# Kernel optimization log

Hardware: AMD Instinct MI355X
Metric: run time of the kernel (lower is better)

Reference implementation:

```python
import jax, jax.numpy as jnp
import numpy as np

N = 20000       # num_nodes
E = 200000      # ~ N*N*0.0005 directed edges from erdos_renyi
IN = 64         # in_channels
HID = 128       # hidden_channels (per head)
H = 4           # heads
OUT = 10        # out_channels
K1 = 10000      # ceil(0.5*N) nodes kept by pool1 (single graph -> static)
K2 = 5000       # ceil(0.5*K1) kept by pool2
NEG_SLOPE = 0.2 # PyG GATConv default negative_slope


def setup_inputs() -> dict:
    key = jax.random.key(0)
    ks = jax.random.split(key, 16)
    def glorot(k, shp, fan):
        return (jax.random.normal(k, shp, jnp.float32) / np.sqrt(fan)).astype(jnp.float32)
    x = jax.random.normal(ks[0], (N, IN), jnp.float32)
    edge_index = jax.random.randint(ks[1], (2, E), 0, N, dtype=jnp.int32)
    batch = jnp.zeros((N,), jnp.int32)
    W1 = glorot(ks[2], (IN, H * HID), IN)
    a_src1 = glorot(ks[3], (H, HID), HID)
    a_dst1 = glorot(ks[4], (H, HID), HID)
    b1 = jnp.zeros((H * HID,), jnp.float32)
    pw1 = glorot(ks[5], (H * HID,), H * HID)
    W2 = glorot(ks[6], (H * HID, H * HID), H * HID)
    a_src2 = glorot(ks[7], (H, HID), HID)
    a_dst2 = glorot(ks[8], (H, HID), HID)
    b2 = jnp.zeros((H * HID,), jnp.float32)
    pw2 = glorot(ks[9], (H * HID,), H * HID)
    Wl = glorot(ks[10], (H * HID, OUT), H * HID)
    bl = jnp.zeros((OUT,), jnp.float32)
    return dict(x=x, edge_index=edge_index, batch=batch,
                W1=W1, a_src1=a_src1, a_dst1=a_dst1, b1=b1, pw1=pw1,
                W2=W2, a_src2=a_src2, a_dst2=a_dst2, b2=b2, pw2=pw2,
                Wl=Wl, bl=bl)


def _gat(x, src, dst, emask, W, a_src, a_dst, bias):
    """PyG GATConv: gather -> LeakyReLU edge score -> scatter-softmax over dst -> scatter-add.
    Self-loops added (PyG default). emask marks valid edges (invalid edges point at node 0)."""
    n = x.shape[0]
    Hh, C = a_src.shape
    h = (x @ W).reshape(n, Hh, C)                      # [n,H,C]
    asrc = jnp.einsum('nhc,hc->nh', h, a_src)          # [n,H]
    adst = jnp.einsum('nhc,hc->nh', h, a_dst)
    loops = jnp.arange(n, dtype=src.dtype)
    sa = jnp.concatenate([src, loops])                 # [E+n]
    da = jnp.concatenate([dst, loops])
    ma = jnp.concatenate([emask, jnp.ones((n,), bool)])
    logit = jax.nn.leaky_relu(asrc[sa] + adst[da], negative_slope=NEG_SLOPE)  # [E+n,H]
    logit = jnp.where(ma[:, None], logit, -1e9)
    mx = jax.ops.segment_max(logit, da, num_segments=n)        # every node has a self-loop
    e = jnp.where(ma[:, None], jnp.exp(logit - mx[da]), 0.0)
    den = jax.ops.segment_sum(e, da, num_segments=n)
    alpha = e / den[da]                                         # [E+n,H]
    msg = (alpha[:, :, None] * h[sa]).reshape(-1, Hh * C)       # [E+n,H*C]
    return jax.ops.segment_sum(msg, da, num_segments=n) + bias  # concat heads + bias


def _topk_pool(x, src, dst, emask, w, k):
    """PyG TopKPooling (single graph): score = tanh(x.w/||w||), keep top-k nodes,
    scale kept features by score, relabel & mask edges between kept nodes."""
    score = jnp.tanh((x @ w) / jnp.linalg.norm(w))     # [n]
    vals, perm = jax.lax.top_k(score, k)
    xn = x[perm] * vals[:, None]                       # [k,F]
    remap = jnp.full((x.shape[0],), -1, jnp.int32).at[perm].set(jnp.arange(k, dtype=jnp.int32))
    s2 = remap[src]
    d2 = remap[dst]
    m2 = emask & (s2 >= 0) & (d2 >= 0)
    return xn, jnp.where(m2, s2, 0), jnp.where(m2, d2, 0), m2


def reference(x, edge_index, batch, W1, a_src1, a_dst1, b1, pw1,
              W2, a_src2, a_dst2, b2, pw2, Wl, bl):
    src = edge_index[0]
    dst = edge_index[1]
    mask = jnp.ones((src.shape[0],), bool)
    h = jax.nn.elu(_gat(x, src, dst, mask, W1, a_src1, a_dst1, b1))
    h, src, dst, mask = _topk_pool(h, src, dst, mask, pw1, K1)
    h = jax.nn.elu(_gat(h, src, dst, mask, W2, a_src2, a_dst2, b2))
    h, src, dst, mask = _topk_pool(h, src, dst, mask, pw2, K2)
    g = jnp.mean(h, axis=0, keepdims=True)             # global_mean_pool, single graph
    return g @ Wl + bl                                  # [1, OUT]
```

## Files before the change

kernel.cpp:

```cpp
#include <hip/hip_runtime.h>
#include <math.h>

#define N_NODES 20000
#define E_EDGES 200000
#define K1_KEEP 10000
#define K2_KEEP 5000
#define HIDC 128
#define NHEAD 4
#define FDIM 512
#define NEG 0.2f
#define BSTRIDE 64
#define MPAD 10112
#define MPAD1 20096
#define FR_GRID 250
#define FR_RPB 40
#define SSTRIDE 16

typedef _Float16 half8 __attribute__((ext_vector_type(8)));
typedef _Float16 half4 __attribute__((ext_vector_type(4)));
typedef float f32x4 __attribute__((ext_vector_type(4)));

__device__ __forceinline__ float leaky(float x){ return x > 0.f ? x : NEG * x; }
__device__ __forceinline__ float elu(float x){ return x > 0.f ? x : expm1f(x); }
__device__ __forceinline__ unsigned ordkey(float f){
    unsigned u = __float_as_uint(f);
    return (u & 0x80000000u) ? ~u : (u | 0x80000000u);
}

__global__ __launch_bounds__(256) void prep_x(const float* __restrict__ x,
        _Float16* __restrict__ X0, _Float16* __restrict__ X1)
{
    int tid = blockIdx.x * 256 + threadIdx.x;
    int r = tid >> 3, c8 = (tid & 7) << 3;
    half8 v0 = (half8)0, v1 = (half8)0;
    if (r < N_NODES){
        const float4* p = reinterpret_cast<const float4*>(&x[(size_t)r * 64 + c8]);
        float4 x0 = p[0], x1 = p[1];
        float vals[8] = {x0.x, x0.y, x0.z, x0.w, x1.x, x1.y, x1.z, x1.w};
#pragma unroll
        for (int j = 0; j < 8; ++j){
            _Float16 h = (_Float16)vals[j];
            v0[j] = h;
            v1[j] = (_Float16)(vals[j] - (float)h);
        }
    }
    *reinterpret_cast<half8*>(&X0[(size_t)r * 64 + c8]) = v0;
    *reinterpret_cast<half8*>(&X1[(size_t)r * 64 + c8]) = v1;
}

__global__ __launch_bounds__(256) void prep_w1x(const float* __restrict__ W1,
        _Float16* __restrict__ B0, _Float16* __restrict__ B1,
        int* __restrict__ ctmp, int cn,
        const float* __restrict__ cw, float* __restrict__ cinvn)
{
    int bid = blockIdx.x;
    int t = threadIdx.x;
    if (bid < 32){
        __shared__ float tile[32][33];
        int bn = bid & 15, bk = bid >> 4;
        int n0 = bn * 32, k0 = bk * 32;
        int j = t & 31, i0 = t >> 5;
#pragma unroll
        for (int ii = 0; ii < 32; ii += 8)
            tile[i0 + ii][j] = W1[(size_t)(k0 + i0 + ii) * 512 + n0 + j];
        __syncthreads();
#pragma unroll
        for (int ii = 0; ii < 32; ii += 8){
            float v = tile[j][i0 + ii];
            _Float16 h0 = (_Float16)v;
            _Float16 h1 = (_Float16)(v - (float)h0);
            size_t o = (size_t)(n0 + i0 + ii) * 64 + k0 + j;
            B0[o] = h0; B1[o] = h1;
        }
    } else if (bid < 32 + 79){
        int i = (bid - 32) * 256 + t;
        if (i < cn) ctmp[i] = 0;
    } else {
        __shared__ float redc[4];
        float s = cw[t] * cw[t] + cw[t + 256] * cw[t + 256];
#pragma unroll
        for (int off = 32; off > 0; off >>= 1) s += __shfl_xor(s, off);
        if ((t & 63) == 0) redc[t >> 6] = s;
        __syncthreads();
        if (t == 0) *cinvn = rsqrtf(redc[0] + redc[1] + redc[2] + redc[3]);
    }
}

__global__ __launch_bounds__(256) void prep_w2(const float* __restrict__ W2,
        _Float16* __restrict__ B0, _Float16* __restrict__ B1)
{
    __shared__ float tile[32][33];
    int bn = blockIdx.x & 15, bk = blockIdx.x >> 4;
    int n0 = bn * 32, k0 = bk * 32;
    int t = threadIdx.x;
    int j = t & 31, i0 = t >> 5;
#pragma unroll
    for (int ii = 0; ii < 32; ii += 8)
        tile[i0 + ii][j] = W2[(size_t)(k0 + i0 + ii) * 512 + n0 + j];
    __syncthreads();
#pragma unroll
    for (int ii = 0; ii < 32; ii += 8){
        float v = tile[j][i0 + ii];
        _Float16 h0 = (_Float16)v;
        _Float16 h1 = (_Float16)(v - (float)h0);
        size_t o = (size_t)(n0 + i0 + ii) * 512 + k0 + j;
        B0[o] = h0; B1[o] = h1;
    }
}

__global__ __launch_bounds__(256) void prep_a(const float* __restrict__ out1,
        const int* __restrict__ oldi, const float* __restrict__ score,
        _Float16* __restrict__ A0, _Float16* __restrict__ A1)
{
    int tid = blockIdx.x * 256 + threadIdx.x;
    int r = tid >> 6, kq = (tid & 63) << 3;
    half8 v0 = (half8)0, v1 = (half8)0;
    if (r < K1_KEEP){
        int o = oldi[r];
        float sc = score[o];
        const float4* p = reinterpret_cast<const float4*>(&out1[(size_t)o * 512 + kq]);
        float4 x0 = p[0], x1 = p[1];
        float vals[8] = {x0.x, x0.y, x0.z, x0.w, x1.x, x1.y, x1.z, x1.w};
#pragma unroll
        for (int j = 0; j < 8; ++j){
            float v = vals[j] * sc;
            _Float16 h = (_Float16)v;
            v0[j] = h;
            v1[j] = (_Float16)(v - (float)h);
        }
    }
    *reinterpret_cast<half8*>(&A0[(size_t)r * 512 + kq]) = v0;
    *reinterpret_cast<half8*>(&A1[(size_t)r * 512 + kq]) = v1;
}

template<int KK>
__global__ __launch_bounds__(256, 2) void gemm_mfma(
        const _Float16* __restrict__ A0, const _Float16* __restrict__ A1,
        const _Float16* __restrict__ B0, const _Float16* __restrict__ B1,
        const float* __restrict__ avS, const float* __restrict__ avD,
        _Float16* __restrict__ C, float* __restrict__ asrc, float* __restrict__ adst,
        int nrows)
{
    __shared__ _Float16 smem[2][4][128][32];
    int t = threadIdx.x;
    int l = t & 63, w = t >> 6;
    int wr = w >> 1, wc = w & 1;
    int bidn = blockIdx.x & 3, bidm = blockIdx.x >> 2;
    int row0 = bidm * 128, col0 = bidn * 128;

    const _Float16* plane = (w == 0) ? A0 : (w == 1) ? A1 : (w == 2) ? B0 : B1;
    int prow0 = (w < 2) ? row0 : col0;
    int mloc = l >> 2;
    int gsw = (l & 3) ^ (mloc & 3);
    const _Float16* gbase = plane + (size_t)(prow0 + mloc) * KK + gsw * 8;

    f32x4 acc[4][4];
#pragma unroll
    for (int m = 0; m < 4; ++m)
#pragma unroll
        for (int n = 0; n < 4; ++n) acc[m][n] = (f32x4){0.f, 0.f, 0.f, 0.f};

    auto stage = [&](int buf, int chunk){
        const _Float16* src = gbase + chunk * 32;
        char* db = (char*)&smem[buf][w][0][0];
#pragma unroll
        for (int i = 0; i < 8; ++i)
            __builtin_amdgcn_global_load_lds(
                (const __attribute__((address_space(1))) void*)(src + (size_t)i * (KK * 16)),
                (__attribute__((address_space(3))) void*)(db + i * 1024), 16, 0, 0);
    };

    int rb = (l & 15) * 64 + (((l >> 4) ^ (l & 3)) * 16);
    const char* sb = (const char*)smem;

    constexpr int NCH = KK / 32;
    stage(0, 0);
    __syncthreads();
    for (int c = 0; c < NCH; ++c){
        int buf = c & 1;
        if (c < NCH - 1) stage(buf ^ 1, c + 1);
        const char* base = sb + buf * 32768;
        half8 a0[4], a1[4], b0[4], b1[4];
#pragma unroll
        for (int m = 0; m < 4; ++m){
            a0[m] = *(const half8*)(base +         wr * 4096 + m * 1024 + rb);
            a1[m] = *(const half8*)(base +  8192 + wr * 4096 + m * 1024 + rb);
            b0[m] = *(const half8*)(base + 16384 + wc * 4096 + m * 1024 + rb);
            b1[m] = *(const half8*)(base + 24576 + wc * 4096 + m * 1024 + rb);
        }
#pragma unroll
        for (int m = 0; m < 4; ++m)
#pragma unroll
            for (int n = 0; n < 4; ++n)
                acc[m][n] = __builtin_amdgcn_mfma_f32_16x16x32_f16(a0[m], b0[n], acc[m][n], 0, 0, 0);
#pragma unroll
        for (int m = 0; m < 4; ++m)
#pragma unroll
            for (int n = 0; n < 4; ++n)
                acc[m][n] = __builtin_amdgcn_mfma_f32_16x16x32_f16(a0[m], b1[n], acc[m][n], 0, 0, 0);
#pragma unroll
        for (int m = 0; m < 4; ++m)
#pragma unroll
            for (int n = 0; n < 4; ++n)
                acc[m][n] = __builtin_amdgcn_mfma_f32_16x16x32_f16(a1[m], b0[n], acc[m][n], 0, 0, 0);
        __syncthreads();
    }

    int head = bidn;
    const float* asv = avS + head * HIDC + wc * 64;
    const float* adv = avD + head * HIDC + wc * 64;
    int lc = l & 15, lg = l >> 4;
    int rbase = row0 + wr * 64;
    int cbase = col0 + wc * 64;
#pragma unroll
    for (int m = 0; m < 4; ++m){
#pragma unroll
        for (int q = 0; q < 4; ++q){
            int row = rbase + m * 16 + lg * 4 + q;
            bool ok = row < nrows;
            float s = 0.f, d = 0.f;
#pragma unroll
            for (int n = 0; n < 4; ++n){
                float v = acc[m][n][q];
                int cc = n * 16 + lc;
                if (ok) C[(size_t)row * 512 + cbase + cc] = (_Float16)v;
                s += v * asv[cc];
                d += v * adv[cc];
            }
#pragma unroll
            for (int off = 1; off < 16; off <<= 1){
                s += __shfl_xor(s, off);
                d += __shfl_xor(d, off);
            }
            if (ok && lc == 0){
                asrc[row * 8 + head * 2 + wc] = s;
                adst[row * 8 + head * 2 + wc] = d;
            }
        }
    }
}

__global__ void edge_fill(const int* __restrict__ src, const int* __restrict__ dst, int e,
                          int* __restrict__ tmp, int* __restrict__ csr){
    int i = blockIdx.x * 256 + threadIdx.x;
    if (i >= e) return;
    int d = dst[i];
    int pos = atomicAdd(&tmp[d], 1);
    if (pos < BSTRIDE) csr[d * BSTRIDE + pos] = src[i];
}

template<bool FILTER>
__global__ __launch_bounds__(256) void gat_fused(const _Float16* __restrict__ h,
        const float* __restrict__ asrc, const float* __restrict__ adst,
        const int* __restrict__ degs, const int* __restrict__ csr,
        const int* __restrict__ oldi, const int* __restrict__ remap,
        const float* __restrict__ bias, const float* __restrict__ pw,
        const float* __restrict__ invn, float* __restrict__ out,
        float* __restrict__ score, int n)
{
    int node = blockIdx.x * 4 + (threadIdx.x >> 6);
    int lane = threadIdx.x & 63;
    if (node >= n) return;
    int od = FILTER ? oldi[node] : node;
    int deg = degs[od]; if (deg > BSTRIDE) deg = BSTRIDE;
    int e0 = od * BSTRIDE;
    int ph = lane & 3;
    int pe = lane >> 2;
    float adn, sown;
    {
        float2 dv = *reinterpret_cast<const float2*>(&adst[(size_t)node * 8 + ph * 2]);
        float2 sv = *reinterpret_cast<const float2*>(&asrc[(size_t)node * 8 + ph * 2]);
        adn = dv.x + dv.y; sown = sv.x + sv.y;
    }
    float slog = leaky(sown + adn);
    int sreg[4];
    float mx = slog;
#pragma unroll
    for (int blk = 0; blk < 4; ++blk){
        int j = blk * 16 + pe;
        int s = -1;
        if (j < deg){
            s = csr[e0 + j];
            if (FILTER) s = remap[s];
            if (s >= 0){
                float2 v = *reinterpret_cast<const float2*>(&asrc[(size_t)s * 8 + ph * 2]);
                mx = fmaxf(mx, leaky(v.x + v.y + adn));
            }
        }
        sreg[blk] = s;
    }
#pragma unroll
    for (int off = 4; off < 64; off <<= 1) mx = fmaxf(mx, __shfl_xor(mx, off));
    float aexp[4];
    float lsum = 0.f;
#pragma unroll
    for (int blk = 0; blk < 4; ++blk){
        float ex = 0.f;
        int s = sreg[blk];
        if (s >= 0){
            float2 v = *reinterpret_cast<const float2*>(&asrc[(size_t)s * 8 + ph * 2]);
            ex = expf(leaky(v.x + v.y + adn) - mx);
        }
        aexp[blk] = ex;
        lsum += ex;
    }
#pragma unroll
    for (int off = 4; off < 64; off <<= 1) lsum += __shfl_xor(lsum, off);
    float es  = expf(slog - mx);
    float inv = 1.f / (lsum + es);

    int f0 = lane * 8;
    int hf = lane >> 4;
    float invh  = __shfl(inv, hf);
    float aself = __shfl(es, hf) * invh;
    float4 acc0, acc1;
    {
        half8 v = *reinterpret_cast<const half8*>(&h[(size_t)node * FDIM + f0]);
        acc0 = make_float4(aself * (float)v[0], aself * (float)v[1],
                           aself * (float)v[2], aself * (float)v[3]);
        acc1 = make_float4(aself * (float)v[4], aself * (float)v[5],
                           aself * (float)v[6], aself * (float)v[7]);
    }
#pragma unroll
    for (int blk = 0; blk < 4; ++blk){
        int base = blk * 16;
        if (base >= deg) break;
        int cnt = deg - base; if (cnt > 16) cnt = 16;
        for (int e = 0; e < cnt; ++e){
            int s = __shfl(sreg[blk], e * 4);
            if (FILTER && s < 0) continue;
            float al = __shfl(aexp[blk], e * 4 + hf) * invh;
            half8 u = *reinterpret_cast<const half8*>(&h[(size_t)s * FDIM + f0]);
            acc0.x += al * (float)u[0]; acc0.y += al * (float)u[1];
            acc0.z += al * (float)u[2]; acc0.w += al * (float)u[3];
            acc1.x += al * (float)u[4]; acc1.y += al * (float)u[5];
            acc1.z += al * (float)u[6]; acc1.w += al * (float)u[7];
        }
    }
    const float4* bp = reinterpret_cast<const float4*>(&bias[f0]);
    float4 b0 = bp[0], b1 = bp[1];
    float4 o0 = make_float4(elu(acc0.x + b0.x), elu(acc0.y + b0.y),
                            elu(acc0.z + b0.z), elu(acc0.w + b0.w));
    float4 o1 = make_float4(elu(acc1.x + b1.x), elu(acc1.y + b1.y),
                            elu(acc1.z + b1.z), elu(acc1.w + b1.w));
    float4* op = reinterpret_cast<float4*>(&out[(size_t)node * FDIM + f0]);
    op[0] = o0; op[1] = o1;
    const float4* wp = reinterpret_cast<const float4*>(&pw[f0]);
    float4 w0 = wp[0], w1 = wp[1];
    float s = o0.x * w0.x + o0.y * w0.y + o0.z * w0.z + o0.w * w0.w
            + o1.x * w1.x + o1.y * w1.y + o1.z * w1.z + o1.w * w1.w;
#pragma unroll
    for (int off = 32; off > 0; off >>= 1) s += __shfl_xor(s, off);
    if (lane == 0) score[node] = tanhf(s * (*invn));
}


__global__ __launch_bounds__(1024) void sel_init(unsigned* __restrict__ gbins,
                                                 unsigned* __restrict__ meta)
{
    int i = blockIdx.x * 1024 + threadIdx.x;
    if (i < 256 * SSTRIDE) gbins[i] = 0u;
    if (i < 64) meta[i] = 0u;
}

template<int PASS>
__global__ __launch_bounds__(256) void sel_hist(const float* __restrict__ score,
        int n, unsigned* __restrict__ gbins, const unsigned* __restrict__ meta)
{
    __shared__ unsigned h[4][256];
    int t = threadIdx.x, wv = t >> 6;
    for (int i = t; i < 1024; i += 256) ((unsigned*)h)[i] = 0u;
    __syncthreads();
    unsigned pref = 0u, pmask = 0u;
    if (PASS < 3){ pref = meta[0]; pmask = 0xFFFFFFFFu << (PASS * 8 + 8); }
    int base = blockIdx.x * 512 + t;
#pragma unroll
    for (int j = 0; j < 2; ++j){
        int i = base + j * 256;
        if (i < n){
            unsigned key = ordkey(score[i]);
            if ((key & pmask) == pref)
                atomicAdd(&h[wv][(key >> (PASS * 8)) & 255u], 1u);
        }
    }
    __syncthreads();
    unsigned a = h[0][t] + h[1][t] + h[2][t] + h[3][t];
    if (a) atomicAdd(&gbins[t * SSTRIDE], a);
}

__global__ __launch_bounds__(256) void sel_scan(unsigned* __restrict__ gbins,
        unsigned* __restrict__ meta, int pass, unsigned k)
{
    __shared__ unsigned wt[4];
    int t = threadIdx.x, lane = t & 63, wv = t >> 6;
    unsigned c = gbins[t * SSTRIDE];
    gbins[t * SSTRIDE] = 0u;
    unsigned rem  = (pass == 3) ? k  : meta[1];
    unsigned pref = (pass == 3) ? 0u : meta[0];
    unsigned v = c;
#pragma unroll
    for (int off = 1; off < 64; off <<= 1){
        unsigned o = __shfl_down(v, off);
        if (lane + off < 64) v += o;
    }
    if (lane == 0) wt[wv] = v;
    __syncthreads();
#pragma unroll
    for (int q = 0; q < 4; ++q)
        if (q > wv) v += wt[q];
    unsigned nxt = v - c;
    if (v >= rem && nxt < rem){
        meta[0] = pref | ((unsigned)t << (pass * 8));
        meta[1] = rem - nxt;
    }
    if (pass == 0 && t == 0){ meta[16] = 0u; meta[32] = 0u; }
}

__global__ __launch_bounds__(256) void sel_compact(const float* __restrict__ score,
        int n, int k, unsigned* __restrict__ meta,
        int* __restrict__ remap, int* __restrict__ oldidx,
        float* __restrict__ zbuf, int zn,
        const float* __restrict__ w, float* __restrict__ invn)
{
    __shared__ unsigned wsum[4];
    __shared__ unsigned gbaseS, tbaseS;
    __shared__ float red2[4];
    int t = threadIdx.x, lane = t & 63, wv = t >> 6;
    unsigned T = meta[0], ties = meta[1];
    int i0 = blockIdx.x * 512 + t;
    int i1 = i0 + 256;
    unsigned key0 = (i0 < n) ? ordkey(score[i0]) : 0u;
    unsigned key1 = (i1 < n) ? ordkey(score[i1]) : 0u;
    int g0 = (i0 < n && key0 > T) ? 1 : 0, e0 = (i0 < n && key0 == T) ? 1 : 0;
    int g1 = (i1 < n && key1 > T) ? 1 : 0, e1 = (i1 < n && key1 == T) ? 1 : 0;
    unsigned pk = ((unsigned)(g0 + g1) << 16) | (unsigned)(e0 + e1);
    unsigned v = pk;
#pragma unroll
    for (int off = 1; off < 64; off <<= 1){
        unsigned o = __shfl_up(v, off);
        if (lane >= off) v += o;
    }
    if (lane == 63) wsum[wv] = v;
    __syncthreads();
    unsigned wb = 0;
    for (int q = 0; q < wv; ++q) wb += wsum[q];
    unsigned excl = wb + v - pk;
    if (t == 255){
        unsigned tot = wb + v;
        gbaseS = atomicAdd(&meta[16], tot >> 16);
        tbaseS = atomicAdd(&meta[32], tot & 0xFFFFu);
    }
    __syncthreads();
    int gpos = (int)(gbaseS + (excl >> 16));
    int tpos = (int)(tbaseS + (excl & 0xFFFFu));
    int gtot = k - (int)ties;
    if (i0 < n){
        int pos = -1;
        if (g0) pos = gpos;
        else if (e0 && tpos < (int)ties) pos = gtot + tpos;
        if (pos >= 0){ remap[i0] = pos; oldidx[pos] = i0; }
        else remap[i0] = -1;
    }
    gpos += g0; tpos += e0;
    if (i1 < n){
        int pos = -1;
        if (g1) pos = gpos;
        else if (e1 && tpos < (int)ties) pos = gtot + tpos;
        if (pos >= 0){ remap[i1] = pos; oldidx[pos] = i1; }
        else remap[i1] = -1;
    }
    if (w && blockIdx.x == 0){
        float s = w[t] * w[t] + w[t + 256] * w[t + 256];
#pragma unroll
        for (int off = 32; off > 0; off >>= 1) s += __shfl_xor(s, off);
        if (lane == 0) red2[wv] = s;
        __syncthreads();
        if (t == 0) *invn = rsqrtf(red2[0] + red2[1] + red2[2] + red2[3]);
    }
    if (zbuf && blockIdx.x == 0){
        if (t < zn) zbuf[t] = 0.f;
        if (t + 256 < zn) zbuf[t + 256] = 0.f;
    }
}

__global__ __launch_bounds__(512) void final_reduce(const float* __restrict__ x,
        const int* __restrict__ remap, const float* __restrict__ score,
        float* __restrict__ acc, const float* __restrict__ Wl)
{
    __shared__ float gsh[512];
    int t = threadIdx.x;
    int r0 = blockIdx.x * FR_RPB;
    float a = 0.f;
#pragma unroll
    for (int i = 0; i < FR_RPB; i += 4){
        int rr = r0 + i;
        float s0 = (remap[rr + 0] >= 0) ? score[rr + 0] : 0.f;
        float s1 = (remap[rr + 1] >= 0) ? score[rr + 1] : 0.f;
        float s2 = (remap[rr + 2] >= 0) ? score[rr + 2] : 0.f;
        float s3 = (remap[rr + 3] >= 0) ? score[rr + 3] : 0.f;
        float v0 = x[(size_t)(rr + 0) * FDIM + t];
        float v1 = x[(size_t)(rr + 1) * FDIM + t];
        float v2 = x[(size_t)(rr + 2) * FDIM + t];
        float v3 = x[(size_t)(rr + 3) * FDIM + t];
        a += v0 * s0 + v1 * s1 + v2 * s2 + v3 * s3;
    }
    gsh[t] = a;
    __syncthreads();
    int wv = t >> 6, lane = t & 63;
#pragma unroll
    for (int rep = 0; rep < 2; ++rep){
        int w = wv + rep * 8;
        if (w >= 10) break;
        float s = 0.f;
#pragma unroll
        for (int f = 0; f < 8; ++f) s += gsh[lane + f * 64] * Wl[(lane + f * 64) * 10 + w];
#pragma unroll
        for (int off = 32; off > 0; off >>= 1) s += __shfl_xor(s, off);
        if (lane == 0) atomicAdd(&acc[w * 32], s);
    }
}

__global__ __launch_bounds__(64) void final_out(const float* __restrict__ acc,
        const float* __restrict__ bl, float* __restrict__ out)
{
    int t = threadIdx.x;
    if (t < 10) out[t] = acc[t * 32] * (1.0f / K2_KEEP) + bl[t];
}

static inline void run_select(const float* score, int n, int k,
        int* remap, int* oldi, unsigned* gbins, unsigned* meta,
        float* zbuf, int zn, const float* w, float* invn, hipStream_t stream)
{
    int nb = (n + 511) / 512;
    sel_hist<3><<<nb, 256, 0, stream>>>(score, n, gbins, meta);
    sel_scan<<<1, 256, 0, stream>>>(gbins, meta, 3, (unsigned)k);
    sel_hist<2><<<nb, 256, 0, stream>>>(score, n, gbins, meta);
    sel_scan<<<1, 256, 0, stream>>>(gbins, meta, 2, (unsigned)k);
    sel_hist<1><<<nb, 256, 0, stream>>>(score, n, gbins, meta);
    sel_scan<<<1, 256, 0, stream>>>(gbins, meta, 1, (unsigned)k);
    sel_hist<0><<<nb, 256, 0, stream>>>(score, n, gbins, meta);
    sel_scan<<<1, 256, 0, stream>>>(gbins, meta, 0, (unsigned)k);
    sel_compact<<<nb, 256, 0, stream>>>(score, n, k, meta, remap, oldi,
                                        zbuf, zn, w, invn);
}

extern "C" void kernel_launch(void* const* d_in, const int* in_sizes, int n_in,
                              void* d_out, int out_size, void* d_ws, size_t ws_size,
                              hipStream_t stream)
{
    (void)in_sizes; (void)n_in; (void)out_size; (void)ws_size;
    const float* x   = (const float*)d_in[0];
    const int*   ei  = (const int*)  d_in[1];
    const float* W1  = (const float*)d_in[3];
    const float* as1 = (const float*)d_in[4];
    const float* ad1 = (const float*)d_in[5];
    const float* b1  = (const float*)d_in[6];
    const float* pw1 = (const float*)d_in[7];
    const float* W2  = (const float*)d_in[8];
    const float* as2 = (const float*)d_in[9];
    const float* ad2 = (const float*)d_in[10];
    const float* b2  = (const float*)d_in[11];
    const float* pw2 = (const float*)d_in[12];
    const float* Wl  = (const float*)d_in[13];
    const float* bl  = (const float*)d_in[14];
    const int* src1 = ei;
    const int* dst1 = ei + E_EDGES;

    char* wsb = (char*)d_ws;
    size_t off = 0;
    auto alloc = [&](size_t bytes) -> char* {
        char* p = wsb + off;
        off += (bytes + 255) & ~(size_t)255;
        return p;
    };
    _Float16* h1f = (_Float16*)alloc((size_t)N_NODES * FDIM * 2);
    float* out1 = (float*)alloc((size_t)N_NODES * FDIM * 4);
    float* asrc = (float*)alloc((size_t)N_NODES * 8 * 4);
    float* adst = (float*)alloc((size_t)N_NODES * 8 * 4);
    float* score= (float*)alloc((size_t)N_NODES * 4);
    float* invn = (float*)alloc(4);
    int* tmp  = (int*)alloc((size_t)N_NODES * 4);
    int* csr  = (int*)alloc((size_t)N_NODES * BSTRIDE * 4);
    int* remap= (int*)alloc((size_t)N_NODES * 4);
    int* oldi = (int*)alloc((size_t)K1_KEEP * 4);
    float* racc = (float*)alloc(320 * 4);
    unsigned* gbins = (unsigned*)alloc(256 * SSTRIDE * 4);
    unsigned* smeta = (unsigned*)alloc(64 * 4);
    _Float16* a0p = (_Float16*)alloc((size_t)MPAD * FDIM * 2);
    _Float16* a1p = (_Float16*)alloc((size_t)MPAD * FDIM * 2);
    _Float16* w2t0 = (_Float16*)alloc((size_t)FDIM * FDIM * 2);
    _Float16* w2t1 = (_Float16*)alloc((size_t)FDIM * FDIM * 2);
    _Float16* x0p = (_Float16*)alloc((size_t)MPAD1 * 64 * 2);
    _Float16* x1p = (_Float16*)alloc((size_t)MPAD1 * 64 * 2);
    _Float16* w1t0 = (_Float16*)alloc((size_t)FDIM * 64 * 2);
    _Float16* w1t1 = (_Float16*)alloc((size_t)FDIM * 64 * 2);
    _Float16* h2f = h1f;
    float* out2 = out1;

    sel_init<<<4, 1024, 0, stream>>>(gbins, smeta);
    prep_x<<<MPAD1 * 8 / 256, 256, 0, stream>>>(x, x0p, x1p);
    prep_w1x<<<112, 256, 0, stream>>>(W1, w1t0, w1t1, tmp, N_NODES, pw1, invn);
    gemm_mfma<64><<<(MPAD1 / 128) * 4, 256, 0, stream>>>(x0p, x1p, w1t0, w1t1,
            as1, ad1, h1f, asrc, adst, N_NODES);
    prep_w2<<<256, 256, 0, stream>>>(W2, w2t0, w2t1);
    edge_fill<<<(E_EDGES + 255) / 256, 256, 0, stream>>>(src1, dst1, E_EDGES, tmp, csr);
    gat_fused<false><<<(N_NODES + 3) / 4, 256, 0, stream>>>(h1f, asrc, adst, tmp, csr,
            nullptr, nullptr, b1, pw1, invn, out1, score, N_NODES);

    run_select(score, N_NODES, K1_KEEP, remap, oldi, gbins, smeta,
               nullptr, 0, pw2, invn, stream);

    prep_a<<<MPAD / 4, 256, 0, stream>>>(out1, oldi, score, a0p, a1p);
    gemm_mfma<512><<<(MPAD / 128) * 4, 256, 0, stream>>>(a0p, a1p, w2t0, w2t1,
            as2, ad2, h2f, asrc, adst, K1_KEEP);
    gat_fused<true><<<(K1_KEEP + 3) / 4, 256, 0, stream>>>(h2f, asrc, adst, tmp, csr,
            oldi, remap, b2, pw2, invn, out2, score, K1_KEEP);

    run_select(score, K1_KEEP, K2_KEEP, remap, oldi, gbins, smeta,
               racc, 320, nullptr, nullptr, stream);
    final_reduce<<<FR_GRID, 512, 0, stream>>>(out2, remap, score, racc, Wl);
    final_out<<<1, 64, 0, stream>>>(racc, bl, (float*)d_out);
}
```

Measured before the change: 274.5 us.

## Fuse radix top-k selection passes into one kernel with grid barriers

Replaces the nine-launch radix select sequence (four histogram and scan pairs plus compact) with a single persistent kernel that uses software grid barriers between passes. Each block keeps its two keys in registers across passes instead of reloading scores. This removes eight kernel launches per selection, and there are two selections. It relies on all blocks (40 or 20) being co-resident, otherwise the spin barrier deadlocks, and it reuses meta slots 48 and 56 as barrier counters.

```diff
diff --git a/kernel.cpp b/kernel.cpp
--- a/kernel.cpp
+++ b/kernel.cpp
@@ -26,6 +26,12 @@
     unsigned u = __float_as_uint(f);
     return (u & 0x80000000u) ? ~u : (u | 0x80000000u);
 }
+__device__ __forceinline__ unsigned aload(const unsigned* p){
+    return __hip_atomic_load(p, __ATOMIC_RELAXED, __HIP_MEMORY_SCOPE_AGENT);
+}
+__device__ __forceinline__ void astore(unsigned* p, unsigned v){
+    __hip_atomic_store(p, v, __ATOMIC_RELAXED, __HIP_MEMORY_SCOPE_AGENT);
+}
 
 __global__ __launch_bounds__(256) void prep_x(const float* __restrict__ x,
         _Float16* __restrict__ X0, _Float16* __restrict__ X1)
@@ -354,83 +360,80 @@
     if (lane == 0) score[node] = tanhf(s * (*invn));
 }
 
-
-__global__ __launch_bounds__(1024) void sel_init(unsigned* __restrict__ gbins,
-                                                 unsigned* __restrict__ meta)
-{
-    int i = blockIdx.x * 1024 + threadIdx.x;
-    if (i < 256 * SSTRIDE) gbins[i] = 0u;
-    if (i < 64) meta[i] = 0u;
-}
-
-template<int PASS>
-__global__ __launch_bounds__(256) void sel_hist(const float* __restrict__ score,
-        int n, unsigned* __restrict__ gbins, const unsigned* __restrict__ meta)
-{
-    __shared__ unsigned h[4][256];
-    int t = threadIdx.x, wv = t >> 6;
-    for (int i = t; i < 1024; i += 256) ((unsigned*)h)[i] = 0u;
-    __syncthreads();
-    unsigned pref = 0u, pmask = 0u;
-    if (PASS < 3){ pref = meta[0]; pmask = 0xFFFFFFFFu << (PASS * 8 + 8); }
-    int base = blockIdx.x * 512 + t;
-#pragma unroll
-    for (int j = 0; j < 2; ++j){
-        int i = base + j * 256;
-        if (i < n){
-            unsigned key = ordkey(score[i]);
-            if ((key & pmask) == pref)
-                atomicAdd(&h[wv][(key >> (PASS * 8)) & 255u], 1u);
-        }
-    }
-    __syncthreads();
-    unsigned a = h[0][t] + h[1][t] + h[2][t] + h[3][t];
-    if (a) atomicAdd(&gbins[t * SSTRIDE], a);
-}
-
-__global__ __launch_bounds__(256) void sel_scan(unsigned* __restrict__ gbins,
-        unsigned* __restrict__ meta, int pass, unsigned k)
-{
-    __shared__ unsigned wt[4];
-    int t = threadIdx.x, lane = t & 63, wv = t >> 6;
-    unsigned c = gbins[t * SSTRIDE];
-    gbins[t * SSTRIDE] = 0u;
-    unsigned rem  = (pass == 3) ? k  : meta[1];
-    unsigned pref = (pass == 3) ? 0u : meta[0];
-    unsigned v = c;
-#pragma unroll
-    for (int off = 1; off < 64; off <<= 1){
-        unsigned o = __shfl_down(v, off);
-        if (lane + off < 64) v += o;
-    }
-    if (lane == 0) wt[wv] = v;
-    __syncthreads();
-#pragma unroll
-    for (int q = 0; q < 4; ++q)
-        if (q > wv) v += wt[q];
-    unsigned nxt = v - c;
-    if (v >= rem && nxt < rem){
-        meta[0] = pref | ((unsigned)t << (pass * 8));
-        meta[1] = rem - nxt;
-    }
-    if (pass == 0 && t == 0){ meta[16] = 0u; meta[32] = 0u; }
-}
-
-__global__ __launch_bounds__(256) void sel_compact(const float* __restrict__ score,
-        int n, int k, unsigned* __restrict__ meta,
-        int* __restrict__ remap, int* __restrict__ oldidx,
+__global__ __launch_bounds__(256) void select_fused(const float* __restrict__ score,
+        int n, int k, int nb, int* __restrict__ remap, int* __restrict__ oldidx,
+        unsigned* __restrict__ gbins, unsigned* __restrict__ meta,
         float* __restrict__ zbuf, int zn,
         const float* __restrict__ w, float* __restrict__ invn)
 {
-    __shared__ unsigned wsum[4];
+    __shared__ unsigned h[4][256];
+    __shared__ unsigned wt[4];
     __shared__ unsigned gbaseS, tbaseS;
     __shared__ float red2[4];
     int t = threadIdx.x, lane = t & 63, wv = t >> 6;
-    unsigned T = meta[0], ties = meta[1];
-    int i0 = blockIdx.x * 512 + t;
-    int i1 = i0 + 256;
+    int bid = blockIdx.x;
+    int i0 = bid * 512 + t, i1 = i0 + 256;
     unsigned key0 = (i0 < n) ? ordkey(score[i0]) : 0u;
     unsigned key1 = (i1 < n) ? ordkey(score[i1]) : 0u;
+
+    auto gbar = [&](){
+        __syncthreads();
+        if (t == 0){
+            __threadfence();
+            unsigned g = aload(&meta[56]);
+            if (atomicAdd(&meta[48], 1u) == (unsigned)(nb - 1)){
+                astore(&meta[48], 0u);
+                __hip_atomic_store(&meta[56], g + 1u, __ATOMIC_RELEASE,
+                                   __HIP_MEMORY_SCOPE_AGENT);
+            } else {
+                while (__hip_atomic_load(&meta[56], __ATOMIC_ACQUIRE,
+                                         __HIP_MEMORY_SCOPE_AGENT) == g)
+                    __builtin_amdgcn_s_sleep(8);
+            }
+        }
+        __syncthreads();
+    };
+
+    for (int pass = 3; pass >= 0; --pass){
+        unsigned pref = 0u, pmask = 0u;
+        if (pass < 3){ pref = aload(&meta[0]); pmask = 0xFFFFFFFFu << (pass * 8 + 8); }
+        for (int i = t; i < 1024; i += 256) ((unsigned*)h)[i] = 0u;
+        __syncthreads();
+        if (i0 < n && (key0 & pmask) == pref)
+            atomicAdd(&h[wv][(key0 >> (pass * 8)) & 255u], 1u);
+        if (i1 < n && (key1 & pmask) == pref)
+            atomicAdd(&h[wv][(key1 >> (pass * 8)) & 255u], 1u);
+        __syncthreads();
+        unsigned a = h[0][t] + h[1][t] + h[2][t] + h[3][t];
+        if (a) atomicAdd(&gbins[t * SSTRIDE], a);
+        gbar();
+        if (bid == 0){
+            unsigned c = aload(&gbins[t * SSTRIDE]);
+            astore(&gbins[t * SSTRIDE], 0u);
+            unsigned rem  = (pass == 3) ? (unsigned)k : aload(&meta[1]);
+            unsigned prf2 = (pass == 3) ? 0u : aload(&meta[0]);
+            unsigned v = c;
+#pragma unroll
+            for (int off = 1; off < 64; off <<= 1){
+                unsigned o = __shfl_down(v, off);
+                if (lane + off < 64) v += o;
+            }
+            if (lane == 0) wt[wv] = v;
+            __syncthreads();
+#pragma unroll
+            for (int q = 0; q < 4; ++q)
+                if (q > wv) v += wt[q];
+            unsigned nxt = v - c;
+            if (v >= rem && nxt < rem){
+                astore(&meta[0], prf2 | ((unsigned)t << (pass * 8)));
+                astore(&meta[1], rem - nxt);
+            }
+            if (pass == 0 && t == 0){ astore(&meta[16], 0u); astore(&meta[32], 0u); }
+        }
+        gbar();
+    }
+
+    unsigned T = aload(&meta[0]), ties = aload(&meta[1]);
     int g0 = (i0 < n && key0 > T) ? 1 : 0, e0 = (i0 < n && key0 == T) ? 1 : 0;
     int g1 = (i1 < n && key1 > T) ? 1 : 0, e1 = (i1 < n && key1 == T) ? 1 : 0;
     unsigned pk = ((unsigned)(g0 + g1) << 16) | (unsigned)(e0 + e1);
@@ -440,10 +443,10 @@
         unsigned o = __shfl_up(v, off);
         if (lane >= off) v += o;
     }
-    if (lane == 63) wsum[wv] = v;
+    if (lane == 63) wt[wv] = v;
     __syncthreads();
     unsigned wb = 0;
-    for (int q = 0; q < wv; ++q) wb += wsum[q];
+    for (int q = 0; q < wv; ++q) wb += wt[q];
     unsigned excl = wb + v - pk;
     if (t == 255){
         unsigned tot = wb + v;
@@ -469,18 +472,28 @@
         if (pos >= 0){ remap[i1] = pos; oldidx[pos] = i1; }
         else remap[i1] = -1;
     }
-    if (w && blockIdx.x == 0){
-        float s = w[t] * w[t] + w[t + 256] * w[t + 256];
-#pragma unroll
-        for (int off = 32; off > 0; off >>= 1) s += __shfl_xor(s, off);
-        if (lane == 0) red2[wv] = s;
-        __syncthreads();
-        if (t == 0) *invn = rsqrtf(red2[0] + red2[1] + red2[2] + red2[3]);
-    }
-    if (zbuf && blockIdx.x == 0){
-        if (t < zn) zbuf[t] = 0.f;
-        if (t + 256 < zn) zbuf[t + 256] = 0.f;
-    }
+    if (bid == 0){
+        if (w){
+            float s = w[t] * w[t] + w[t + 256] * w[t + 256];
+#pragma unroll
+            for (int off = 32; off > 0; off >>= 1) s += __shfl_xor(s, off);
+            if (lane == 0) red2[wv] = s;
+            __syncthreads();
+            if (t == 0) *invn = rsqrtf(red2[0] + red2[1] + red2[2] + red2[3]);
+        }
+        if (zbuf){
+            if (t < zn) zbuf[t] = 0.f;
+            if (t + 256 < zn) zbuf[t + 256] = 0.f;
+        }
+    }
+}
+
+__global__ __launch_bounds__(1024) void sel_init(unsigned* __restrict__ gbins,
+                                                 unsigned* __restrict__ meta)
+{
+    int i = blockIdx.x * 1024 + threadIdx.x;
+    if (i < 256 * SSTRIDE) gbins[i] = 0u;
+    if (i < 64) meta[i] = 0u;
 }
 
 __global__ __launch_bounds__(512) void final_reduce(const float* __restrict__ x,
@@ -525,23 +538,6 @@
 {
     int t = threadIdx.x;
     if (t < 10) out[t] = acc[t * 32] * (1.0f / K2_KEEP) + bl[t];
-}
-
-static inline void run_select(const float* score, int n, int k,
-        int* remap, int* oldi, unsigned* gbins, unsigned* meta,
-        float* zbuf, int zn, const float* w, float* invn, hipStream_t stream)
-{
-    int nb = (n + 511) / 512;
-    sel_hist<3><<<nb, 256, 0, stream>>>(score, n, gbins, meta);
-    sel_scan<<<1, 256, 0, stream>>>(gbins, meta, 3, (unsigned)k);
-    sel_hist<2><<<nb, 256, 0, stream>>>(score, n, gbins, meta);
-    sel_scan<<<1, 256, 0, stream>>>(gbins, meta, 2, (unsigned)k);
-    sel_hist<1><<<nb, 256, 0, stream>>>(score, n, gbins, meta);
-    sel_scan<<<1, 256, 0, stream>>>(gbins, meta, 1, (unsigned)k);
-    sel_hist<0><<<nb, 256, 0, stream>>>(score, n, gbins, meta);
-    sel_scan<<<1, 256, 0, stream>>>(gbins, meta, 0, (unsigned)k);
-    sel_compact<<<nb, 256, 0, stream>>>(score, n, k, meta, remap, oldi,
-                                        zbuf, zn, w, invn);
 }
 
 extern "C" void kernel_launch(void* const* d_in, const int* in_sizes, int n_in,
@@ -607,8 +603,11 @@
     gat_fused<false><<<(N_NODES + 3) / 4, 256, 0, stream>>>(h1f, asrc, adst, tmp, csr,
             nullptr, nullptr, b1, pw1, invn, out1, score, N_NODES);
 
-    run_select(score, N_NODES, K1_KEEP, remap, oldi, gbins, smeta,
-               nullptr, 0, pw2, invn, stream);
+    {
+        int nb = (N_NODES + 511) / 512;
+        select_fused<<<nb, 256, 0, stream>>>(score, N_NODES, K1_KEEP, nb,
+                remap, oldi, gbins, smeta, nullptr, 0, pw2, invn);
+    }
 
     prep_a<<<MPAD / 4, 256, 0, stream>>>(out1, oldi, score, a0p, a1p);
     gemm_mfma<512><<<(MPAD / 128) * 4, 256, 0, stream>>>(a0p, a1p, w2t0, w2t1,
@@ -616,8 +615,11 @@
     gat_fused<true><<<(K1_KEEP + 3) / 4, 256, 0, stream>>>(h2f, asrc, adst, tmp, csr,
             oldi, remap, b2, pw2, invn, out2, score, K1_KEEP);
 
-    run_select(score, K1_KEEP, K2_KEEP, remap, oldi, gbins, smeta,
-               racc, 320, nullptr, nullptr, stream);
+    {
+        int nb = (K1_KEEP + 511) / 512;
+        select_fused<<<nb, 256, 0, stream>>>(score, K1_KEEP, K2_KEEP, nb,
+                remap, oldi, gbins, smeta, racc, 320, nullptr, nullptr);
+    }
     final_reduce<<<FR_GRID, 512, 0, stream>>>(out2, remap, score, racc, Wl);
     final_out<<<1, 64, 0, stream>>>(racc, bl, (float*)d_out);
 }
```

Result: slower. 302.6 us (+10.2%).
